# Kernel optimization log

Hardware: AMD Instinct MI355X
Metric: run time of the kernel (lower is better)

The kernel has to match this reference:

```python
import math
import jax, jax.numpy as jnp
import numpy as np

B, T, H, E, K, F = 4, 4096, 512, 8, 2, 2048
CAP_FACTOR, ROUND_TO = 0.3125, 128


def _capacity(num_tokens):
    cap = math.ceil(CAP_FACTOR * num_tokens)
    cap = ROUND_TO * math.ceil(cap / ROUND_TO)
    return max(1, min(cap, num_tokens))


def setup_inputs() -> dict:
    key = jax.random.key(0)
    k0, k1, k2, k3 = jax.random.split(key, 4)
    x = jax.random.normal(k0, (B, T, H), jnp.float32)
    router_w = jax.random.normal(k1, (H, E), jnp.float32) * 0.02
    w1 = jax.random.normal(k2, (E, H, F), jnp.float32) * (1.0 / np.sqrt(H))
    b1 = jnp.zeros((E, F), jnp.float32)
    w2 = jax.random.normal(k3, (E, F, H), jnp.float32) * (1.0 / np.sqrt(F))
    b2 = jnp.zeros((E, H), jnp.float32)
    return {"x": x, "router_w": router_w, "w1": w1, "b1": b1, "w2": w2, "b2": b2}


def reference(x, router_w, w1, b1, w2, b2):
    Bc, Tc, Hc = x.shape
    n = Bc * Tc
    cap = _capacity(n)  # static: 5120
    flat = x.reshape(n, Hc)

    # Router + top-k selection (fp32 logits, softmax over selected logits)
    logits = (flat @ router_w).astype(jnp.float32)          # [n, E]
    sel_logits, expert_idx = jax.lax.top_k(logits, K)       # [n, K]
    weights = jax.nn.softmax(sel_logits, axis=-1)           # [n, K]

    # Flatten (token, k) assignments and sort by expert (stable)
    fe = expert_idx.reshape(-1).astype(jnp.int32)           # [n*K]
    fw = weights.reshape(-1)
    tok = jnp.broadcast_to(jnp.arange(n, dtype=jnp.int32)[:, None], expert_idx.shape).reshape(-1)
    order = jnp.argsort(fe)  # jax sort is stable
    se, st, sw = fe[order], tok[order], fw[order]

    # Per-expert slot index; assignments beyond capacity are dropped
    counts = jnp.bincount(se, length=E)                     # [E]
    offsets = (jnp.cumsum(counts) - counts).astype(jnp.int32)
    slot = jnp.arange(se.shape[0], dtype=jnp.int32) - offsets[se]
    keep = slot < cap
    sw = jnp.where(keep, sw, 0.0)                           # dropped tokens contribute 0

    # Pack into fixed-capacity expert buffers (out-of-range slots dropped)
    sx = flat[st]                                           # [n*K, H]
    expert_inputs = jnp.zeros((E, cap, Hc), flat.dtype).at[se, slot].set(sx, mode='drop')

    # Grouped expert MLP: Dense(F) -> GELU -> Dense(H)
    h = jax.nn.gelu(jnp.einsum('ech,ehf->ecf', expert_inputs, w1) + b1[:, None, :])
    out = jnp.einsum('ecf,efh->ech', h, w2) + b2[:, None, :]

    # Zero invalid (unused) slots
    clipped = jnp.minimum(counts, cap)
    valid = (jnp.arange(cap, dtype=jnp.int32)[None, :] < clipped[:, None])[..., None]
    out = jnp.where(valid, out, 0)

    # Scatter-combine weighted expert outputs back to tokens
    slot_c = jnp.minimum(slot, cap - 1)                     # dropped rows have weight 0
    gathered = out[se, slot_c] * sw[:, None].astype(out.dtype)
    combined = jnp.zeros((n, Hc), out.dtype).at[st].add(gathered)
    return combined.reshape(Bc, Tc, Hc)
```

## Files before the change

### kernel.cpp

```cpp
#include <hip/hip_runtime.h>
#include <hip/hip_bf16.h>

#define NTOK 16384
#define HD   512
#define ED   8
#define FD   2048
#define CAP  5120
#define NA   32768

typedef __bf16 bf16x8 __attribute__((ext_vector_type(8)));
typedef float  f32x4  __attribute__((ext_vector_type(4)));

static constexpr size_t OFF_EIDX = 0;
static constexpr size_t OFF_WGT  = 131072;
static constexpr size_t OFF_STOK = 262144;
static constexpr size_t OFF_SWGT = 458752;
static constexpr size_t OFF_W2T  = 1u << 20;
static constexpr size_t OFF_H    = OFF_W2T + (size_t)ED*HD*FD*2;
static constexpr size_t OFF_W1T  = OFF_H   + (size_t)ED*CAP*FD*2;
static constexpr size_t OFF_XBF  = OFF_W1T + (size_t)ED*FD*HD*2;

__device__ __forceinline__ unsigned short f2bf(float f) {
    __bf16 b = (__bf16)f;
    return __builtin_bit_cast(unsigned short, b);
}

__device__ __forceinline__ float gelu_fast(float v) {
    const float u = 1.5957691216057308f * (v + 0.044715f * v * v * v);
    return v / (1.f + __expf(-u));
}

__global__ __launch_bounds__(256) void transpose_cast_kernel(
    const float* __restrict__ in, unsigned short* __restrict__ out, int R, int C)
{
    __shared__ unsigned short tile[32][33];
    const int e = blockIdx.z;
    in  += (size_t)e * R * C;
    out += (size_t)e * R * C;
    const int r0 = blockIdx.y * 32, c0 = blockIdx.x * 32;
    const int tr = threadIdx.x >> 3, tc = (threadIdx.x & 7) * 4;
    const float4 v = *(const float4*)(in + (size_t)(r0 + tr) * C + c0 + tc);
    tile[tr][tc + 0] = f2bf(v.x);
    tile[tr][tc + 1] = f2bf(v.y);
    tile[tr][tc + 2] = f2bf(v.z);
    tile[tr][tc + 3] = f2bf(v.w);
    __syncthreads();
    ushort4 o;
    o.x = tile[tc + 0][tr]; o.y = tile[tc + 1][tr];
    o.z = tile[tc + 2][tr]; o.w = tile[tc + 3][tr];
    *(ushort4*)(out + (size_t)(c0 + tr) * R + r0 + tc) = o;
}

__global__ __launch_bounds__(256) void router_kernel(
    const float* __restrict__ x, const float* __restrict__ rw,
    int* __restrict__ eidx, float* __restrict__ wgt,
    unsigned short* __restrict__ xbf)
{
    __shared__ float rws[HD * ED];
    const int tid = threadIdx.x;
    for (int i = tid * 4; i < HD * ED; i += 256 * 4)
        *(float4*)(rws + i) = *(const float4*)(rw + i);
    __syncthreads();

    const int wid = tid >> 6, lane = tid & 63;
    const int t = blockIdx.x * 4 + wid;
    const float* xr = x + (size_t)t * HD;

    float acc[ED];
#pragma unroll
    for (int e = 0; e < ED; e++) acc[e] = 0.f;

    float4 xv0 = *(const float4*)(xr + lane * 8);
    float4 xv1 = *(const float4*)(xr + lane * 8 + 4);
    float xv[8] = {xv0.x, xv0.y, xv0.z, xv0.w, xv1.x, xv1.y, xv1.z, xv1.w};

    union { unsigned short us[8]; uint4 v; } pk;
#pragma unroll
    for (int j = 0; j < 8; j++) pk.us[j] = f2bf(xv[j]);
    *(uint4*)(xbf + (size_t)t * HD + lane * 8) = pk.v;

#pragma unroll
    for (int j = 0; j < 8; j++) {
        const int h = lane * 8 + j;
#pragma unroll
        for (int e = 0; e < ED; e++) acc[e] += xv[j] * rws[h * ED + e];
    }
#pragma unroll
    for (int off = 32; off >= 1; off >>= 1) {
#pragma unroll
        for (int e = 0; e < ED; e++) acc[e] += __shfl_down(acc[e], off);
    }
    if (lane == 0) {
        int e0 = 0; float l0 = acc[0];
        for (int e = 1; e < ED; e++) if (acc[e] > l0) { l0 = acc[e]; e0 = e; }
        int e1 = 0; float l1 = -1e30f;
        for (int e = 0; e < ED; e++) {
            if (e == e0) continue;
            if (acc[e] > l1) { l1 = acc[e]; e1 = e; }
        }
        const float ex = expf(l1 - l0);
        const float inv = 1.f / (1.f + ex);
        eidx[t * 2 + 0] = e0;  eidx[t * 2 + 1] = e1;
        wgt [t * 2 + 0] = inv; wgt [t * 2 + 1] = ex * inv;
    }
}

__global__ __launch_bounds__(1024) void scan_kernel(
    const int* __restrict__ eidx, const float* __restrict__ wgt,
    int* __restrict__ stok, float* __restrict__ swgt)
{
    __shared__ int running[ED];
    __shared__ int wcnt[16][ED];
    const int tid = threadIdx.x;

    for (int i = tid; i < ED * CAP; i += 1024) stok[i] = -1;
    if (tid < ED) running[tid] = 0;
    __syncthreads();

    const int lane = tid & 63, wid = tid >> 6;
    const unsigned long long below = (1ull << lane) - 1ull;

    for (int c = 0; c < NA / 1024; c++) {
        const int a = c * 1024 + tid;
        const int e = eidx[a];
        const float w = wgt[a];
        int myrank = 0;
#pragma unroll
        for (int ee = 0; ee < ED; ee++) {
            unsigned long long m = __ballot(e == ee);
            if (ee == e) myrank = __popcll(m & below);
            if (lane == 0) wcnt[wid][ee] = __popcll(m);
        }
        __syncthreads();
        int woff = 0;
        for (int ww = 0; ww < wid; ww++) woff += wcnt[ww][e];
        const int slot = running[e] + woff + myrank;
        if (slot < CAP) {
            stok[e * CAP + slot] = a >> 1;
            swgt[e * CAP + slot] = w;
        }
        __syncthreads();
        if (tid < ED) {
            int tot = 0;
            for (int ww = 0; ww < 16; ww++) tot += wcnt[ww][tid];
            running[tid] += tot;
        }
        __syncthreads();
    }
}

template<int KD, int ND, int NT, bool FUSE>
__global__ __launch_bounds__(256) void gemm_mfma(
    const unsigned short* __restrict__ Abase,
    const unsigned short* __restrict__ Bt,
    const float* __restrict__ bias,
    const int* __restrict__ stok,
    const float* __restrict__ swgt,
    unsigned short* __restrict__ hout,
    float* __restrict__ out)
{
    constexpr int RS   = 40;
    constexpr int BUFE = 128 * RS;
    __shared__ __align__(16) unsigned short As[2 * BUFE];
    __shared__ __align__(16) unsigned short Bs[2 * BUFE];

    const int tid = threadIdx.x;
    const int e  = blockIdx.x & 7;
    const int g  = blockIdx.x >> 3;
    const int n0 = (g % NT) * 128;
    const int m0 = (g / NT) * 128;

    const int q  = tid & 3;
    const int r1 = tid >> 2;
    const int r2 = r1 + 64;

    size_t ai1, ai2;
    if (!FUSE) {
        const int t1 = stok[e * CAP + m0 + r1];
        const int t2 = stok[e * CAP + m0 + r2];
        ai1 = (size_t)(t1 >= 0 ? t1 : 0);
        ai2 = (size_t)(t2 >= 0 ? t2 : 0);
    } else {
        ai1 = (size_t)(e * CAP + m0 + r1);
        ai2 = (size_t)(e * CAP + m0 + r2);
    }
    const unsigned short* arow1 = Abase + ai1 * KD + q * 8;
    const unsigned short* arow2 = Abase + ai2 * KD + q * 8;
    const unsigned short* brow1 = Bt + ((size_t)e * ND + n0 + r1) * KD + q * 8;
    const unsigned short* brow2 = Bt + ((size_t)e * ND + n0 + r2) * KD + q * 8;

    const int oW1 = r1 * RS + q * 8;
    const int oW2 = r2 * RS + q * 8;

    const int lane = tid & 63;
    const int wid  = tid >> 6;
    const int wrow = (wid & 1) * 64;
    const int wcol = (wid >> 1) * 64;
    const int l15  = lane & 15;
    const int quad = lane >> 4;
    const int fA   = (wrow + l15) * RS + quad * 8;
    const int fB   = (wcol + l15) * RS + quad * 8;

    f32x4 acc[4][4];
#pragma unroll
    for (int i = 0; i < 4; i++)
#pragma unroll
        for (int j = 0; j < 4; j++) acc[i][j] = (f32x4)0.f;

    float4 ra1 = *(const float4*)(arow1);
    float4 ra2 = *(const float4*)(arow2);
    float4 rb1 = *(const float4*)(brow1);
    float4 rb2 = *(const float4*)(brow2);
    *(float4*)(&As[oW1]) = ra1;
    *(float4*)(&As[oW2]) = ra2;
    *(float4*)(&Bs[oW1]) = rb1;
    *(float4*)(&Bs[oW2]) = rb2;
    if (32 < KD) {
        ra1 = *(const float4*)(arow1 + 32);
        ra2 = *(const float4*)(arow2 + 32);
        rb1 = *(const float4*)(brow1 + 32);
        rb2 = *(const float4*)(brow2 + 32);
    }
    __syncthreads();

#define COMPUTE(PBUF)                                                          \
    {                                                                          \
        const unsigned short* Ab = As + (PBUF) * BUFE;                         \
        const unsigned short* Bb = Bs + (PBUF) * BUFE;                         \
        bf16x8 af[4], bfv[4];                                                  \
        _Pragma("unroll")                                                      \
        for (int i = 0; i < 4; i++) af[i]  = *(const bf16x8*)(Ab + fA + i * 16 * RS); \
        _Pragma("unroll")                                                      \
        for (int j = 0; j < 4; j++) bfv[j] = *(const bf16x8*)(Bb + fB + j * 16 * RS); \
        _Pragma("unroll")                                                      \
        for (int i = 0; i < 4; i++)                                            \
            _Pragma("unroll")                                                  \
            for (int j = 0; j < 4; j++)                                        \
                acc[i][j] = __builtin_amdgcn_mfma_f32_16x16x32_bf16(           \
                    af[i], bfv[j], acc[i][j], 0, 0, 0);                        \
    }

    int rbuf = 0;
    for (int kc = 0; kc < KD; kc += 32) {
        const int wb = (rbuf ^ 1) * BUFE;
        if (kc + 32 < KD) {
            *(float4*)(&As[wb + oW1]) = ra1;
            *(float4*)(&As[wb + oW2]) = ra2;
            *(float4*)(&Bs[wb + oW1]) = rb1;
            *(float4*)(&Bs[wb + oW2]) = rb2;
            if (kc + 64 < KD) {
                ra1 = *(const float4*)(arow1 + kc + 64);
                ra2 = *(const float4*)(arow2 + kc + 64);
                rb1 = *(const float4*)(brow1 + kc + 64);
                rb2 = *(const float4*)(brow2 + kc + 64);
            }
        }
        COMPUTE(rbuf);
        __syncthreads();
        rbuf ^= 1;
    }
#undef COMPUTE

    if (!FUSE) {
#pragma unroll
        for (int i = 0; i < 4; i++) {
#pragma unroll
            for (int g2 = 0; g2 < 4; g2++) {
                const int m = wrow + i * 16 + quad * 4 + g2;
                unsigned short* hrow = hout + ((size_t)e * CAP + m0 + m) * FD + n0;
#pragma unroll
                for (int j = 0; j < 4; j++) {
                    const int n = wcol + j * 16 + l15;
                    const float v = acc[i][j][g2] + bias[(size_t)e * ND + n0 + n];
                    hrow[n] = f2bf(gelu_fast(v));
                }
            }
        }
    } else {
#pragma unroll
        for (int i = 0; i < 4; i++) {
#pragma unroll
            for (int g2 = 0; g2 < 4; g2++) {
                const int m = wrow + i * 16 + quad * 4 + g2;
                const int tok = stok[e * CAP + m0 + m];
                if (tok >= 0) {
                    const float w = swgt[e * CAP + m0 + m];
                    float* orow = out + (size_t)tok * HD + n0;
#pragma unroll
                    for (int j = 0; j < 4; j++) {
                        const int n = wcol + j * 16 + l15;
                        const float v = (acc[i][j][g2] + bias[(size_t)e * ND + n0 + n]) * w;
                        atomicAdd(orow + n, v);
                    }
                }
            }
        }
    }
}

extern "C" void kernel_launch(void* const* d_in, const int* in_sizes, int n_in,
                              void* d_out, int out_size, void* d_ws, size_t ws_size,
                              hipStream_t stream)
{
    const float* x  = (const float*)d_in[0];
    const float* rw = (const float*)d_in[1];
    const float* w1 = (const float*)d_in[2];
    const float* b1 = (const float*)d_in[3];
    const float* w2 = (const float*)d_in[4];
    const float* b2 = (const float*)d_in[5];
    float* out = (float*)d_out;

    char* ws = (char*)d_ws;
    int*   eidx = (int*)  (ws + OFF_EIDX);
    float* wgt  = (float*)(ws + OFF_WGT);
    int*   stok = (int*)  (ws + OFF_STOK);
    float* swgt = (float*)(ws + OFF_SWGT);
    unsigned short* w2t  = (unsigned short*)(ws + OFF_W2T);
    unsigned short* hbuf = (unsigned short*)(ws + OFF_H);
    unsigned short* w1t  = (unsigned short*)(ws + OFF_W1T);
    unsigned short* xbf  = (unsigned short*)(ws + OFF_XBF);

    transpose_cast_kernel<<<dim3(FD / 32, HD / 32, ED), 256, 0, stream>>>(w1, w1t, HD, FD);
    transpose_cast_kernel<<<dim3(HD / 32, FD / 32, ED), 256, 0, stream>>>(w2, w2t, FD, HD);
    router_kernel<<<NTOK / 4, 256, 0, stream>>>(x, rw, eidx, wgt, xbf);
    scan_kernel<<<1, 1024, 0, stream>>>(eidx, wgt, stok, swgt);
    hipMemsetAsync(d_out, 0, (size_t)out_size * sizeof(float), stream);

    gemm_mfma<HD, FD, FD/128, false>
        <<<8 * (FD/128) * (CAP/128), 256, 0, stream>>>(
        xbf, w1t, b1, stok, nullptr, hbuf, nullptr);

    gemm_mfma<FD, HD, HD/128, true>
        <<<8 * (HD/128) * (CAP/128), 256, 0, stream>>>(
        hbuf, w2t, b2, stok, swgt, nullptr, out);
}
```

Measured before the change: 520.3 us.

## Use direct global-to-LDS loads with swizzle and replace atomic combine with gather kernel

The GEMM staging now uses global_load_lds to copy tiles straight into an unpadded, XOR-swizzled shared-memory layout, and the launch bounds request higher occupancy. The second GEMM no longer scatters weighted results to tokens with float atomics. Instead it writes per-slot expert outputs in fp16, and a new combine kernel gathers each token's two slots and applies the routing weights. This removes atomic contention and the output memset, at the cost of an extra intermediate buffer round trip and fp16 rounding of expert outputs.

```diff
diff --git a/kernel.cpp b/kernel.cpp
--- a/kernel.cpp
+++ b/kernel.cpp
@@ -14,20 +14,34 @@
 static constexpr size_t OFF_EIDX = 0;
 static constexpr size_t OFF_WGT  = 131072;
 static constexpr size_t OFF_STOK = 262144;
-static constexpr size_t OFF_SWGT = 458752;
+static constexpr size_t OFF_ASLOT= 425984;
 static constexpr size_t OFF_W2T  = 1u << 20;
 static constexpr size_t OFF_H    = OFF_W2T + (size_t)ED*HD*FD*2;
 static constexpr size_t OFF_W1T  = OFF_H   + (size_t)ED*CAP*FD*2;
 static constexpr size_t OFF_XBF  = OFF_W1T + (size_t)ED*FD*HD*2;
+static constexpr size_t OFF_EOUT = OFF_XBF + (size_t)NTOK*HD*2;
 
 __device__ __forceinline__ unsigned short f2bf(float f) {
     __bf16 b = (__bf16)f;
     return __builtin_bit_cast(unsigned short, b);
 }
+__device__ __forceinline__ unsigned short f2h(float f) {
+    _Float16 h = (_Float16)f;
+    return __builtin_bit_cast(unsigned short, h);
+}
+__device__ __forceinline__ float h2f(unsigned short u) {
+    return (float)__builtin_bit_cast(_Float16, u);
+}
 
 __device__ __forceinline__ float gelu_fast(float v) {
     const float u = 1.5957691216057308f * (v + 0.044715f * v * v * v);
     return v / (1.f + __expf(-u));
+}
+
+__device__ __forceinline__ void gl16(const unsigned short* g, unsigned short* l) {
+    __builtin_amdgcn_global_load_lds(
+        (const __attribute__((address_space(1))) unsigned int*)(const void*)g,
+        (__attribute__((address_space(3))) unsigned int*)(void*)l, 16, 0, 0);
 }
 
 __global__ __launch_bounds__(256) void transpose_cast_kernel(
@@ -106,8 +120,8 @@
 }
 
 __global__ __launch_bounds__(1024) void scan_kernel(
-    const int* __restrict__ eidx, const float* __restrict__ wgt,
-    int* __restrict__ stok, float* __restrict__ swgt)
+    const int* __restrict__ eidx,
+    int* __restrict__ stok, int* __restrict__ aslot)
 {
     __shared__ int running[ED];
     __shared__ int wcnt[16][ED];
@@ -123,7 +137,6 @@
     for (int c = 0; c < NA / 1024; c++) {
         const int a = c * 1024 + tid;
         const int e = eidx[a];
-        const float w = wgt[a];
         int myrank = 0;
 #pragma unroll
         for (int ee = 0; ee < ED; ee++) {
@@ -137,7 +150,9 @@
         const int slot = running[e] + woff + myrank;
         if (slot < CAP) {
             stok[e * CAP + slot] = a >> 1;
-            swgt[e * CAP + slot] = w;
+            aslot[a] = slot;
+        } else {
+            aslot[a] = -1;
         }
         __syncthreads();
         if (tid < ED) {
@@ -149,18 +164,15 @@
     }
 }
 
-template<int KD, int ND, int NT, bool FUSE>
-__global__ __launch_bounds__(256) void gemm_mfma(
+template<int KD, int ND, int NT, bool G1>
+__global__ __launch_bounds__(256, 5) void gemm_mfma(
     const unsigned short* __restrict__ Abase,
     const unsigned short* __restrict__ Bt,
     const float* __restrict__ bias,
     const int* __restrict__ stok,
-    const float* __restrict__ swgt,
-    unsigned short* __restrict__ hout,
-    float* __restrict__ out)
-{
-    constexpr int RS   = 40;
-    constexpr int BUFE = 128 * RS;
+    unsigned short* __restrict__ hout)
+{
+    constexpr int BUFE = 128 * 32;
     __shared__ __align__(16) unsigned short As[2 * BUFE];
     __shared__ __align__(16) unsigned short Bs[2 * BUFE];
 
@@ -170,36 +182,41 @@
     const int n0 = (g % NT) * 128;
     const int m0 = (g / NT) * 128;
 
-    const int q  = tid & 3;
-    const int r1 = tid >> 2;
-    const int r2 = r1 + 64;
-
-    size_t ai1, ai2;
-    if (!FUSE) {
-        const int t1 = stok[e * CAP + m0 + r1];
-        const int t2 = stok[e * CAP + m0 + r2];
-        ai1 = (size_t)(t1 >= 0 ? t1 : 0);
-        ai2 = (size_t)(t2 >= 0 ? t2 : 0);
-    } else {
-        ai1 = (size_t)(e * CAP + m0 + r1);
-        ai2 = (size_t)(e * CAP + m0 + r2);
-    }
-    const unsigned short* arow1 = Abase + ai1 * KD + q * 8;
-    const unsigned short* arow2 = Abase + ai2 * KD + q * 8;
-    const unsigned short* brow1 = Bt + ((size_t)e * ND + n0 + r1) * KD + q * 8;
-    const unsigned short* brow2 = Bt + ((size_t)e * ND + n0 + r2) * KD + q * 8;
-
-    const int oW1 = r1 * RS + q * 8;
-    const int oW2 = r2 * RS + q * 8;
-
     const int lane = tid & 63;
     const int wid  = tid >> 6;
+
+    const int rsub = lane >> 2;
+    const int csw  = (lane & 3) ^ ((rsub >> 1) & 3);
+
+    const unsigned short *ag0, *ag1, *bg0, *bg1;
+    {
+        const int R0 = (wid * 2 + 0) * 16 + rsub;
+        const int R1 = (wid * 2 + 1) * 16 + rsub;
+        size_t a0, a1;
+        if constexpr (G1) {
+            const int t0 = stok[e * CAP + m0 + R0];
+            const int t1 = stok[e * CAP + m0 + R1];
+            a0 = (size_t)(t0 >= 0 ? t0 : 0);
+            a1 = (size_t)(t1 >= 0 ? t1 : 0);
+        } else {
+            a0 = (size_t)(e * CAP + m0 + R0);
+            a1 = (size_t)(e * CAP + m0 + R1);
+        }
+        ag0 = Abase + a0 * KD + csw * 8;
+        ag1 = Abase + a1 * KD + csw * 8;
+        bg0 = Bt + ((size_t)e * ND + n0 + R0) * KD + csw * 8;
+        bg1 = Bt + ((size_t)e * ND + n0 + R1) * KD + csw * 8;
+    }
+    unsigned short* lA = As + (wid * 2) * 512;
+    unsigned short* lB = Bs + (wid * 2) * 512;
+
     const int wrow = (wid & 1) * 64;
     const int wcol = (wid >> 1) * 64;
     const int l15  = lane & 15;
     const int quad = lane >> 4;
-    const int fA   = (wrow + l15) * RS + quad * 8;
-    const int fB   = (wcol + l15) * RS + quad * 8;
+    const int xq   = quad ^ ((l15 >> 1) & 3);
+    const int fA   = (wrow + l15) * 32 + xq * 8;
+    const int fB   = (wcol + l15) * 32 + xq * 8;
 
     f32x4 acc[4][4];
 #pragma unroll
@@ -207,31 +224,23 @@
 #pragma unroll
         for (int j = 0; j < 4; j++) acc[i][j] = (f32x4)0.f;
 
-    float4 ra1 = *(const float4*)(arow1);
-    float4 ra2 = *(const float4*)(arow2);
-    float4 rb1 = *(const float4*)(brow1);
-    float4 rb2 = *(const float4*)(brow2);
-    *(float4*)(&As[oW1]) = ra1;
-    *(float4*)(&As[oW2]) = ra2;
-    *(float4*)(&Bs[oW1]) = rb1;
-    *(float4*)(&Bs[oW2]) = rb2;
-    if (32 < KD) {
-        ra1 = *(const float4*)(arow1 + 32);
-        ra2 = *(const float4*)(arow2 + 32);
-        rb1 = *(const float4*)(brow1 + 32);
-        rb2 = *(const float4*)(brow2 + 32);
-    }
-    __syncthreads();
-
-#define COMPUTE(PBUF)                                                          \
+#define STAGE(B, KC)                                                           \
     {                                                                          \
-        const unsigned short* Ab = As + (PBUF) * BUFE;                         \
-        const unsigned short* Bb = Bs + (PBUF) * BUFE;                         \
+        gl16(ag0 + (KC), lA + (B) * BUFE);                                     \
+        gl16(ag1 + (KC), lA + (B) * BUFE + 512);                               \
+        gl16(bg0 + (KC), lB + (B) * BUFE);                                     \
+        gl16(bg1 + (KC), lB + (B) * BUFE + 512);                               \
+    }
+
+#define COMPUTE(B)                                                             \
+    {                                                                          \
+        const unsigned short* Ab = As + (B) * BUFE;                            \
+        const unsigned short* Bb = Bs + (B) * BUFE;                            \
         bf16x8 af[4], bfv[4];                                                  \
         _Pragma("unroll")                                                      \
-        for (int i = 0; i < 4; i++) af[i]  = *(const bf16x8*)(Ab + fA + i * 16 * RS); \
+        for (int i = 0; i < 4; i++) af[i]  = *(const bf16x8*)(Ab + fA + i * 512); \
         _Pragma("unroll")                                                      \
-        for (int j = 0; j < 4; j++) bfv[j] = *(const bf16x8*)(Bb + fB + j * 16 * RS); \
+        for (int j = 0; j < 4; j++) bfv[j] = *(const bf16x8*)(Bb + fB + j * 512); \
         _Pragma("unroll")                                                      \
         for (int i = 0; i < 4; i++)                                            \
             _Pragma("unroll")                                                  \
@@ -240,62 +249,63 @@
                     af[i], bfv[j], acc[i][j], 0, 0, 0);                        \
     }
 
-    int rbuf = 0;
-    for (int kc = 0; kc < KD; kc += 32) {
-        const int wb = (rbuf ^ 1) * BUFE;
-        if (kc + 32 < KD) {
-            *(float4*)(&As[wb + oW1]) = ra1;
-            *(float4*)(&As[wb + oW2]) = ra2;
-            *(float4*)(&Bs[wb + oW1]) = rb1;
-            *(float4*)(&Bs[wb + oW2]) = rb2;
-            if (kc + 64 < KD) {
-                ra1 = *(const float4*)(arow1 + kc + 64);
-                ra2 = *(const float4*)(arow2 + kc + 64);
-                rb1 = *(const float4*)(brow1 + kc + 64);
-                rb2 = *(const float4*)(brow2 + kc + 64);
+    STAGE(0, 0);
+    __syncthreads();
+
+    for (int kc = 0; kc <= KD - 128; kc += 64) {
+        STAGE(1, kc + 32);
+        COMPUTE(0);
+        __syncthreads();
+        STAGE(0, kc + 64);
+        COMPUTE(1);
+        __syncthreads();
+    }
+    STAGE(1, KD - 32);
+    COMPUTE(0);
+    __syncthreads();
+    COMPUTE(1);
+#undef STAGE
+#undef COMPUTE
+
+#pragma unroll
+    for (int i = 0; i < 4; i++) {
+#pragma unroll
+        for (int g2 = 0; g2 < 4; g2++) {
+            const int m = wrow + i * 16 + quad * 4 + g2;
+            unsigned short* hrow = hout + ((size_t)e * CAP + m0 + m) * ND + n0;
+#pragma unroll
+            for (int j = 0; j < 4; j++) {
+                const int n = wcol + j * 16 + l15;
+                const float v = acc[i][j][g2] + bias[(size_t)e * ND + n0 + n];
+                hrow[n] = G1 ? f2bf(gelu_fast(v)) : f2h(v);
             }
         }
-        COMPUTE(rbuf);
-        __syncthreads();
-        rbuf ^= 1;
-    }
-#undef COMPUTE
-
-    if (!FUSE) {
-#pragma unroll
-        for (int i = 0; i < 4; i++) {
-#pragma unroll
-            for (int g2 = 0; g2 < 4; g2++) {
-                const int m = wrow + i * 16 + quad * 4 + g2;
-                unsigned short* hrow = hout + ((size_t)e * CAP + m0 + m) * FD + n0;
-#pragma unroll
-                for (int j = 0; j < 4; j++) {
-                    const int n = wcol + j * 16 + l15;
-                    const float v = acc[i][j][g2] + bias[(size_t)e * ND + n0 + n];
-                    hrow[n] = f2bf(gelu_fast(v));
-                }
-            }
-        }
-    } else {
-#pragma unroll
-        for (int i = 0; i < 4; i++) {
-#pragma unroll
-            for (int g2 = 0; g2 < 4; g2++) {
-                const int m = wrow + i * 16 + quad * 4 + g2;
-                const int tok = stok[e * CAP + m0 + m];
-                if (tok >= 0) {
-                    const float w = swgt[e * CAP + m0 + m];
-                    float* orow = out + (size_t)tok * HD + n0;
-#pragma unroll
-                    for (int j = 0; j < 4; j++) {
-                        const int n = wcol + j * 16 + l15;
-                        const float v = (acc[i][j][g2] + bias[(size_t)e * ND + n0 + n]) * w;
-                        atomicAdd(orow + n, v);
-                    }
-                }
-            }
-        }
-    }
+    }
+}
+
+__global__ __launch_bounds__(256) void combine_kernel(
+    const unsigned short* __restrict__ eout,
+    const int* __restrict__ eidx, const int* __restrict__ aslot,
+    const float* __restrict__ wgt, float* __restrict__ out)
+{
+    const int tid = threadIdx.x;
+    const int t  = blockIdx.x * 2 + (tid >> 7);
+    const int h0 = (tid & 127) * 4;
+    float r0 = 0.f, r1 = 0.f, r2 = 0.f, r3 = 0.f;
+#pragma unroll
+    for (int k = 0; k < 2; k++) {
+        const int a = t * 2 + k;
+        const int s = aslot[a];
+        if (s >= 0) {
+            const float w = wgt[a];
+            const int e = eidx[a];
+            const ushort4 v = *(const ushort4*)(eout + ((size_t)e * CAP + s) * HD + h0);
+            r0 += w * h2f(v.x); r1 += w * h2f(v.y);
+            r2 += w * h2f(v.z); r3 += w * h2f(v.w);
+        }
+    }
+    float4 o; o.x = r0; o.y = r1; o.z = r2; o.w = r3;
+    *(float4*)(out + (size_t)t * HD + h0) = o;
 }
 
 extern "C" void kernel_launch(void* const* d_in, const int* in_sizes, int n_in,
@@ -311,26 +321,28 @@
     float* out = (float*)d_out;
 
     char* ws = (char*)d_ws;
-    int*   eidx = (int*)  (ws + OFF_EIDX);
-    float* wgt  = (float*)(ws + OFF_WGT);
-    int*   stok = (int*)  (ws + OFF_STOK);
-    float* swgt = (float*)(ws + OFF_SWGT);
+    int*   eidx  = (int*)  (ws + OFF_EIDX);
+    float* wgt   = (float*)(ws + OFF_WGT);
+    int*   stok  = (int*)  (ws + OFF_STOK);
+    int*   aslot = (int*)  (ws + OFF_ASLOT);
     unsigned short* w2t  = (unsigned short*)(ws + OFF_W2T);
     unsigned short* hbuf = (unsigned short*)(ws + OFF_H);
     unsigned short* w1t  = (unsigned short*)(ws + OFF_W1T);
     unsigned short* xbf  = (unsigned short*)(ws + OFF_XBF);
+    unsigned short* eout = (unsigned short*)(ws + OFF_EOUT);
 
     transpose_cast_kernel<<<dim3(FD / 32, HD / 32, ED), 256, 0, stream>>>(w1, w1t, HD, FD);
     transpose_cast_kernel<<<dim3(HD / 32, FD / 32, ED), 256, 0, stream>>>(w2, w2t, FD, HD);
     router_kernel<<<NTOK / 4, 256, 0, stream>>>(x, rw, eidx, wgt, xbf);
-    scan_kernel<<<1, 1024, 0, stream>>>(eidx, wgt, stok, swgt);
-    hipMemsetAsync(d_out, 0, (size_t)out_size * sizeof(float), stream);
-
-    gemm_mfma<HD, FD, FD/128, false>
+    scan_kernel<<<1, 1024, 0, stream>>>(eidx, stok, aslot);
+
+    gemm_mfma<HD, FD, FD/128, true>
         <<<8 * (FD/128) * (CAP/128), 256, 0, stream>>>(
-        xbf, w1t, b1, stok, nullptr, hbuf, nullptr);
-
-    gemm_mfma<FD, HD, HD/128, true>
+        xbf, w1t, b1, stok, hbuf);
+
+    gemm_mfma<FD, HD, HD/128, false>
         <<<8 * (HD/128) * (CAP/128), 256, 0, stream>>>(
-        hbuf, w2t, b2, stok, swgt, nullptr, out);
-}
+        hbuf, w2t, b2, nullptr, eout);
+
+    combine_kernel<<<NTOK / 2, 256, 0, stream>>>(eout, eidx, aslot, wgt, out);
+}
```

Result: slower. 714.4 us (+37.3%).
